# Optimization experiments

Measured on AMD Instinct MI355X. Metric: run time of the kernel, lower is better.

The kernel has to match this reference:

```python
import jax, jax.numpy as jnp
import numpy as np

B, FEAT, Q, L, H_ENC, H_DEC = 256, 64, 16, 2, 128, 256


def _apply_1q(state, U, q):
    # state: [B, 2,2,...,2] (Q qubit axes); U: [B,2,2] complex64
    s = jnp.moveaxis(state, 1 + q, 1)
    shp = s.shape
    s2 = s.reshape(shp[0], 2, -1)
    s2 = jnp.einsum('bij,bjr->bir', U, s2)
    return jnp.moveaxis(s2.reshape(shp), 1, 1 + q)


def _apply_cnot(state, c, t):
    # flip target axis on the control=1 slice
    c0 = jnp.take(state, 0, axis=1 + c)
    c1 = jnp.take(state, 1, axis=1 + c)
    t_ax = 1 + t if t < c else t  # target axis index after removing control axis
    c1 = jnp.flip(c1, axis=t_ax)
    return jnp.stack([c0, c1], axis=1 + c)


def _u3(theta, phi, lam):
    # combined Rz(lam) @ Ry(phi) @ Rx(theta); inputs [B] -> [B,2,2] complex64
    j = jnp.complex64(1j)
    ct, st = jnp.cos(theta / 2), jnp.sin(theta / 2)
    cp, sp = jnp.cos(phi / 2), jnp.sin(phi / 2)
    Rx = jnp.stack([jnp.stack([ct + 0j, -j * st], -1),
                    jnp.stack([-j * st, ct + 0j], -1)], -2)
    Ry = jnp.stack([jnp.stack([cp + 0j, -sp + 0j], -1),
                    jnp.stack([sp + 0j, cp + 0j], -1)], -2)
    em, ep = jnp.exp(-j * lam / 2), jnp.exp(j * lam / 2)
    zero = jnp.zeros_like(em)
    Rz = jnp.stack([jnp.stack([em, zero], -1),
                    jnp.stack([zero, ep], -1)], -2)
    return jnp.einsum('bij,bjk,bkl->bil', Rz, Ry, Rx).astype(jnp.complex64)


def setup_inputs() -> dict:
    key = jax.random.key(0)
    ks = jax.random.split(key, 6)

    def xavier(k, shape):
        lim = float(np.sqrt(6.0 / (shape[0] + shape[1])))
        return jax.random.uniform(k, shape, jnp.float32, -lim, lim)

    return {
        'x': jax.random.normal(ks[0], (B, FEAT), jnp.float32),
        'W1': xavier(ks[1], (FEAT, H_ENC)), 'b1': jnp.zeros((H_ENC,), jnp.float32),
        'W2': xavier(ks[2], (H_ENC, L * Q * 3)), 'b2': jnp.zeros((L * Q * 3,), jnp.float32),
        'scaling': jnp.ones((Q,), jnp.float32),
        'Wd1': xavier(ks[3], (2 ** Q, H_DEC)), 'bd1': jnp.zeros((H_DEC,), jnp.float32),
        'Wd2': xavier(ks[4], (H_DEC, FEAT)), 'bd2': jnp.zeros((FEAT,), jnp.float32),
    }


def reference(x, W1, b1, W2, b2, scaling, Wd1, bd1, Wd2, bd2):
    batch = x.shape[0]
    nq = scaling.shape[0]
    nl = W2.shape[1] // (nq * 3)
    # classical encoder -> quantum rotation angles
    h = jax.nn.relu(x @ W1 + b1)
    p = jnp.tanh(h @ W2 + b2).reshape(batch, nl, nq, 3)
    p = p * scaling[None, None, :, None] * jnp.pi  # theta/phi/lambda scaled by pi
    # batched statevector simulation, |0...0> init
    state = jnp.zeros((batch, 2 ** nq), jnp.complex64).at[:, 0].set(1.0)
    state = state.reshape((batch,) + (2,) * nq)
    for l in range(nl):
        for q in range(nq):
            U = _u3(p[:, l, q, 0], p[:, l, q, 1], p[:, l, q, 2])
            state = _apply_1q(state, U, q)
        if l < nl - 1:
            for q in range(nq - 1):
                state = _apply_cnot(state, q, q + 1)
            state = _apply_cnot(state, nq - 1, 0)
    probs = (jnp.real(state) ** 2 + jnp.imag(state) ** 2).reshape(batch, -1)
    # classical decoder
    out = jax.nn.relu(jax.nn.relu(probs @ Wd1 + bd1) @ Wd2 + bd2)
    return out
```

## Files before the change

kernel.cpp:

```cpp
#include <hip/hip_runtime.h>
#include <hip/hip_fp16.h>

#define PI_F 3.14159265358979323846f

typedef __attribute__((ext_vector_type(8))) _Float16 f16x8;
typedef __attribute__((ext_vector_type(16))) float f32x16;
typedef __attribute__((ext_vector_type(2))) float v2f;

__device__ __forceinline__ v2f pfma(v2f a, v2f b, v2f c) {
    return __builtin_elementwise_fma(a, b, c);
}
__device__ __forceinline__ v2f vswap(v2f a) { return __builtin_shufflevector(a, a, 1, 0); }
__device__ __forceinline__ v2f vsplat(float x) { v2f r; r.x = x; r.y = x; return r; }
__device__ __forceinline__ v2f mkc(v2f u) { v2f r; r.x = -u.y; r.y = u.y; return r; }
__device__ __forceinline__ v2f cmul(v2f a, v2f b) {
    return pfma(mkc(a), vswap(b), vsplat(a.x) * b);
}

__device__ __forceinline__ unsigned f2bf_rn(float x) {
    unsigned u = __float_as_uint(x);
    return (u + 0x7fffu + ((u >> 16) & 1u)) >> 16;
}

union H8 { int4 i4; f16x8 v; };
union U8 { int4 i4; unsigned short u[8]; };

__device__ __forceinline__ void gll16(const void* g, void* l) {
    __builtin_amdgcn_global_load_lds(
        (const __attribute__((address_space(1))) void*)g,
        (__attribute__((address_space(3))) void*)l, 16, 0, 0);
}

struct PreLds {
    float xr[64]; float h[128]; float ang[96];
    v2f vL[32];
    v2f uL[64];
    _Float16 lR[256*8];
    _Float16 lL[512*8];
};

__global__ __launch_bounds__(512) void k_pre(
        const float* __restrict__ x, const float* __restrict__ W1,
        const float* __restrict__ b1, const float* __restrict__ W2,
        const float* __restrict__ b2, const float* __restrict__ scaling,
        _Float16* __restrict__ A) {
    __shared__ PreLds lds;
    const int t = threadIdx.x;
    const int b = blockIdx.x;
    if (t < 64) lds.xr[t] = x[b*64 + t];
    __syncthreads();
    if (t < 128) {
        float acc = b1[t];
        #pragma unroll 8
        for (int f = 0; f < 64; ++f) acc = fmaf(lds.xr[f], W1[f*128 + t], acc);
        lds.h[t] = fmaxf(acc, 0.f);
    }
    __syncthreads();
    if (t < 96) {
        float acc = b2[t];
        #pragma unroll 8
        for (int f = 0; f < 128; ++f) acc = fmaf(lds.h[f], W2[f*96 + t], acc);
        int q = (t/3) & 15;
        lds.ang[t] = tanhf(acc) * scaling[q] * PI_F;
    }
    __syncthreads();
    if (t < 32) {
        int l = t >> 4, q = t & 15;
        const float* a = lds.ang + l*48 + q*3;
        float st, ct, sp, cp, sl, cl;
        sincosf(a[0]*0.5f, &st, &ct);
        sincosf(a[1]*0.5f, &sp, &cp);
        sincosf(a[2]*0.5f, &sl, &cl);
        float2 A00 = make_float2( cp*ct,  sp*st);
        float2 A01 = make_float2(-sp*ct, -cp*st);
        float2 A10 = make_float2( sp*ct, -cp*st);
        float2 A11 = make_float2( cp*ct, -sp*st);
        float2 e0 = make_float2(cl, -sl), e1 = make_float2(cl, sl);
        v2f r00; r00.x = e0.x*A00.x - e0.y*A00.y; r00.y = e0.x*A00.y + e0.y*A00.x;
        v2f r01; r01.x = e0.x*A01.x - e0.y*A01.y; r01.y = e0.x*A01.y + e0.y*A01.x;
        v2f r10; r10.x = e1.x*A10.x - e1.y*A10.y; r10.y = e1.x*A10.y + e1.y*A10.x;
        v2f r11; r11.x = e1.x*A11.x - e1.y*A11.y; r11.y = e1.x*A11.y + e1.y*A11.x;
        if (l == 0) {
            lds.vL[q*2 + 0] = r00;
            lds.vL[q*2 + 1] = r10;
        } else {
            lds.uL[q*4 + 0] = r00; lds.uL[q*4 + 1] = r01;
            lds.uL[q*4 + 2] = r10; lds.uL[q*4 + 3] = r11;
        }
    }
    __syncthreads();
    #define AP(p, s) lds.vL[(15-(p))*2 + (s)]
    #define GG(p, zv, yv) lds.uL[(15-(p))*4 + (zv)*2 + (yv)]
    {
        const float SL = 32.f;
        if (t < 256) {
            v2f Lg[2][2];
            int z0 = t & 1, z1 = (t >> 1) & 1;
            #pragma unroll
            for (int g = 0; g < 2; ++g)
                #pragma unroll
                for (int y = 0; y < 2; ++y)
                    Lg[g][y] = cmul(cmul(GG(0, z0, g), AP(0, g ^ y)), GG(1, z1, y));
            #pragma unroll
            for (int p = 2; p <= 7; ++p) {
                int zp = (t >> p) & 1;
                #pragma unroll
                for (int g = 0; g < 2; ++g) {
                    v2f s0 = cmul(Lg[g][0], AP(p-1, 0)) + cmul(Lg[g][1], AP(p-1, 1));
                    v2f s1 = cmul(Lg[g][0], AP(p-1, 1)) + cmul(Lg[g][1], AP(p-1, 0));
                    Lg[g][0] = cmul(s0, GG(p, zp, 0));
                    Lg[g][1] = cmul(s1, GG(p, zp, 1));
                }
            }
            float lre[4] = {Lg[0][0].x, Lg[0][1].x, Lg[1][0].x, Lg[1][1].x};
            float lim[4] = {Lg[0][0].y, Lg[0][1].y, Lg[1][0].y, Lg[1][1].y};
            H8 hre, him;
            #pragma unroll
            for (int k = 0; k < 4; ++k) {
                hre.v[k]   = (_Float16)(SL * lre[k]);
                hre.v[4+k] = (_Float16)(-SL * lim[k]);
                him.v[k]   = (_Float16)(SL * lim[k]);
                him.v[4+k] = (_Float16)(SL * lre[k]);
            }
            *(int4*)&lds.lL[t*8]         = hre.i4;
            *(int4*)&lds.lL[(256+t)*8]   = him.i4;
        } else {
            const int ts = t - 256;
            v2f Rg[2][2];
            int z15 = (ts >> 7) & 1;
            #pragma unroll
            for (int g = 0; g < 2; ++g)
                #pragma unroll
                for (int y14 = 0; y14 < 2; ++y14)
                    Rg[g][y14] = cmul(cmul(AP(14, y14 ^ g),     AP(15, g)),     GG(15, z15, 0))
                               + cmul(cmul(AP(14, y14 ^ 1 ^ g), AP(15, 1 ^ g)), GG(15, z15, 1));
            #pragma unroll
            for (int p = 14; p >= 8; --p) {
                int zp = (ts >> (p - 8)) & 1;
                #pragma unroll
                for (int g = 0; g < 2; ++g) {
                    v2f t0 = cmul(GG(p, zp, 0), Rg[g][0]);
                    v2f t1 = cmul(GG(p, zp, 1), Rg[g][1]);
                    v2f n0 = cmul(AP(p-1, 0), t0) + cmul(AP(p-1, 1), t1);
                    v2f n1 = cmul(AP(p-1, 1), t0) + cmul(AP(p-1, 0), t1);
                    Rg[g][0] = n0; Rg[g][1] = n1;
                }
            }
            float rre[4] = {Rg[0][0].x, Rg[0][1].x, Rg[1][0].x, Rg[1][1].x};
            float rim[4] = {Rg[0][0].y, Rg[0][1].y, Rg[1][0].y, Rg[1][1].y};
            H8 hr;
            #pragma unroll
            for (int k = 0; k < 4; ++k) {
                hr.v[k]    = (_Float16)(SL * rre[k]);
                hr.v[4+k]  = (_Float16)(SL * rim[k]);
            }
            *(int4*)&lds.lR[ts*8] = hr.i4;
        }
    }
    #undef AP
    #undef GG
    __syncthreads();
    {
        const int wave = t >> 6, lane = t & 63, h2 = lane >> 5, l32 = lane & 31;
        f16x8 zf = {};
        _Float16* Aout = A + ((size_t)b << 16);
        const int zh0 = wave*32;
        f16x8 rf = h2 ? zf : *(const f16x8*)&lds.lR[(zh0 + l32)*8];
        _Float16* rowp = Aout + (size_t)(zh0 + l32)*256 + 4*h2;
        #pragma unroll
        for (int j = 0; j < 8; ++j) {
            f16x8 bre = h2 ? zf : *(const f16x8*)&lds.lL[(j*32 + l32)*8];
            f16x8 bim = h2 ? zf : *(const f16x8*)&lds.lL[(256 + j*32 + l32)*8];
            f32x16 zc = {};
            f32x16 dre = __builtin_amdgcn_mfma_f32_32x32x16_f16(bre, rf, zc, 0, 0, 0);
            f32x16 dim = __builtin_amdgcn_mfma_f32_32x32x16_f16(bim, rf, zc, 0, 0, 0);
            #pragma unroll
            for (int g = 0; g < 4; ++g) {
                union { _Float16 h4[4]; uint2 u2; } pk;
                #pragma unroll
                for (int i = 0; i < 4; ++i) {
                    int q = g*4 + i;
                    float p = fmaf(dre[q], dre[q], dim[q]*dim[q]) * 0.00390625f;
                    pk.h4[i] = (_Float16)p;
                }
                *(uint2*)(rowp + j*32 + 8*g) = pk.u2;
            }
        }
    }
}

__global__ __launch_bounds__(512, 4) void k_gemm(
        const _Float16* __restrict__ A, const float* __restrict__ Wd1,
        unsigned short* __restrict__ partial) {
    __shared__ _Float16 lA[256*64];
    __shared__ _Float16 lB[64*64];
    const int id = blockIdx.x;
    const int xcd = id & 7;
    const int ksg = xcd*16 + ((id >> 3) & 15);
    const int nh  = id >> 7;
    const int k0 = ksg*512, n0 = nh*64;
    const int tid = threadIdx.x;
    const int wave = tid >> 6, lane = tid & 63;
    const int mw = wave >> 1, nw = wave & 1;
    const int h = lane >> 5, l32 = lane & 31;
    const int kw = tid >> 4;
    const int nc4 = (tid & 15) * 4;
    unsigned* lBw = (unsigned*)lB;
    f32x16 acc[2] = {};
    for (int s = 0; s < 8; ++s) {
        const int kb = k0 + s*64;
        const float* wsrc = Wd1 + (size_t)(kb + 2*kw)*256 + n0 + nc4;
        float4 w0 = *(const float4*)(wsrc);
        float4 w1 = *(const float4*)(wsrc + 256);
        #pragma unroll
        for (int i = 0; i < 4; ++i) {
            int ia = wave*4 + i;
            int r = ia*8 + (lane >> 3);
            int cch = (lane & 7) ^ (r & 7);
            gll16(A + (size_t)r*65536 + kb + cch*8, &lA[ia*512]);
        }
        {
            float a0[4] = {w0.x,w0.y,w0.z,w0.w};
            float a1[4] = {w1.x,w1.y,w1.z,w1.w};
            #pragma unroll
            for (int j = 0; j < 4; ++j) {
                int n = nc4 + j;
                int S = ((n >> 3) & 7) ^ (n & 7);
                __half2 hh = __floats2half2_rn(a0[j]*64.f, a1[j]*64.f);
                unsigned u; __builtin_memcpy(&u, &hh, 4);
                lBw[n*32 + (((kw >> 2) ^ S) << 2) + (kw & 3)] = u;
            }
        }
        __syncthreads();
        #pragma unroll
        for (int kk = 0; kk < 4; ++kk) {
            const int ch = kk*2 + h;
            f16x8 af[2], bf;
            #pragma unroll
            for (int xx = 0; xx < 2; ++xx) {
                int rA = mw*64 + xx*32 + l32;
                af[xx] = *(const f16x8*)&lA[rA*64 + ((ch ^ (rA & 7)) << 3)];
            }
            int rB = nw*32 + l32;
            int SB = ((rB >> 3) & 7) ^ (rB & 7);
            bf = *(const f16x8*)&lB[rB*64 + ((ch ^ SB) << 3)];
            #pragma unroll
            for (int i = 0; i < 2; ++i)
                acc[i] = __builtin_amdgcn_mfma_f32_32x32x16_f16(af[i], bf, acc[i], 0, 0, 0);
        }
        __syncthreads();
    }
    #pragma unroll
    for (int i = 0; i < 2; ++i) {
        int n = n0 + nw*32 + l32;
        int mb = mw*64 + i*32 + 4*h;
        #pragma unroll
        for (int q = 0; q < 16; ++q) {
            int m = mb + (q & 3) + 8*(q >> 2);
            partial[((size_t)m*128 + ksg)*256 + n] = (unsigned short)f2bf_rn(acc[i][q]);
        }
    }
}

__global__ __launch_bounds__(256) void k_final(
        const unsigned short* __restrict__ partial, const float* __restrict__ bd1,
        const float* __restrict__ Wd2, const float* __restrict__ bd2,
        float* __restrict__ out) {
    __shared__ float red[8][256];
    __shared__ float row[256];
    __shared__ float red2[4][64];
    const int m = blockIdx.x, t = threadIdx.x;
    const int o = t & 31, kg = t >> 5;
    {
        const unsigned short* p = partial + (size_t)m*32768 + kg*16*256 + o*8;
        float acc[8] = {0.f,0.f,0.f,0.f,0.f,0.f,0.f,0.f};
        #pragma unroll 8
        for (int i = 0; i < 16; ++i) {
            U8 v; v.i4 = *(const int4*)(p + (size_t)i*256);
            #pragma unroll
            for (int j = 0; j < 8; ++j)
                acc[j] += __uint_as_float(((unsigned)v.u[j]) << 16);
        }
        #pragma unroll
        for (int j = 0; j < 8; ++j) red[kg][o*8 + j] = acc[j];
    }
    __syncthreads();
    {
        float s = 0.f;
        #pragma unroll
        for (int g = 0; g < 8; ++g) s += red[g][t];
        const float SC = 1.f / 262144.f;
        row[t] = fmaxf(fmaf(s, SC, bd1[t]), 0.f);
    }
    __syncthreads();
    {
        const int g = t >> 6, tt = t & 63;
        float o2 = 0.f;
        #pragma unroll 8
        for (int i = 0; i < 64; ++i) {
            int n = g*64 + i;
            o2 = fmaf(row[n], Wd2[n*64 + tt], o2);
        }
        red2[g][tt] = o2;
    }
    __syncthreads();
    if (t < 64) {
        float o3 = bd2[t] + ((red2[0][t] + red2[1][t]) + (red2[2][t] + red2[3][t]));
        out[m*64 + t] = fmaxf(o3, 0.f);
    }
}

extern "C" void kernel_launch(void* const* d_in, const int* in_sizes, int n_in,
                              void* d_out, int out_size, void* d_ws, size_t ws_size,
                              hipStream_t stream) {
    const float* x       = (const float*)d_in[0];
    const float* W1      = (const float*)d_in[1];
    const float* b1      = (const float*)d_in[2];
    const float* W2      = (const float*)d_in[3];
    const float* b2      = (const float*)d_in[4];
    const float* scaling = (const float*)d_in[5];
    const float* Wd1     = (const float*)d_in[6];
    const float* bd1     = (const float*)d_in[7];
    const float* Wd2     = (const float*)d_in[8];
    const float* bd2     = (const float*)d_in[9];
    float* out = (float*)d_out;

    char* ws = (char*)d_ws;
    const size_t MB = 1024*1024;
    _Float16* A  = (_Float16*)(ws + 4*MB);
    unsigned short* partial = (unsigned short*)(ws + 36*MB);

    hipLaunchKernelGGL(k_pre, dim3(256), dim3(512), 0, stream,
                       x, W1, b1, W2, b2, scaling, A);
    hipLaunchKernelGGL(k_gemm, dim3(512), dim3(512), 0, stream, A, Wd1, partial);
    hipLaunchKernelGGL(k_final, dim3(256), dim3(256), 0, stream,
                       partial, bd1, Wd2, bd2, out);
}
```

Measured before the change: 159.7 us.

## Use narrower N tiles and longer K splits in decoder GEMM

Changes the split-K GEMM tiling from 64-wide N tiles with 128 K-splits of 512 to 32-wide N tiles with 64 K-splits of 1024. Each wave now computes one 32x32 MFMA tile instead of two. The partial-sum buffer and the final reduction shrink by half. This cuts partial-buffer traffic and reduction work, at the cost of re-reading the A matrix for each of twice as many N tiles and running a longer per-block K loop.

```diff
diff --git a/kernel.cpp b/kernel.cpp
--- a/kernel.cpp
+++ b/kernel.cpp
@@ -193,25 +193,24 @@
         const _Float16* __restrict__ A, const float* __restrict__ Wd1,
         unsigned short* __restrict__ partial) {
     __shared__ _Float16 lA[256*64];
-    __shared__ _Float16 lB[64*64];
+    __shared__ _Float16 lB[32*64];
     const int id = blockIdx.x;
     const int xcd = id & 7;
-    const int ksg = xcd*16 + ((id >> 3) & 15);
-    const int nh  = id >> 7;
-    const int k0 = ksg*512, n0 = nh*64;
+    const int ksg = xcd*8 + ((id >> 3) & 7);
+    const int nh  = id >> 6;
+    const int k0 = ksg*1024, n0 = nh*32;
     const int tid = threadIdx.x;
     const int wave = tid >> 6, lane = tid & 63;
-    const int mw = wave >> 1, nw = wave & 1;
     const int h = lane >> 5, l32 = lane & 31;
     const int kw = tid >> 4;
-    const int nc4 = (tid & 15) * 4;
+    const int nc = (tid & 15) * 2;
     unsigned* lBw = (unsigned*)lB;
-    f32x16 acc[2] = {};
-    for (int s = 0; s < 8; ++s) {
+    f32x16 acc = {};
+    for (int s = 0; s < 16; ++s) {
         const int kb = k0 + s*64;
-        const float* wsrc = Wd1 + (size_t)(kb + 2*kw)*256 + n0 + nc4;
-        float4 w0 = *(const float4*)(wsrc);
-        float4 w1 = *(const float4*)(wsrc + 256);
+        const float* wsrc = Wd1 + (size_t)(kb + 2*kw)*256 + n0 + nc;
+        float2 w0 = *(const float2*)(wsrc);
+        float2 w1 = *(const float2*)(wsrc + 256);
         #pragma unroll
         for (int i = 0; i < 4; ++i) {
             int ia = wave*4 + i;
@@ -220,11 +219,11 @@
             gll16(A + (size_t)r*65536 + kb + cch*8, &lA[ia*512]);
         }
         {
-            float a0[4] = {w0.x,w0.y,w0.z,w0.w};
-            float a1[4] = {w1.x,w1.y,w1.z,w1.w};
-            #pragma unroll
-            for (int j = 0; j < 4; ++j) {
-                int n = nc4 + j;
+            float a0[2] = {w0.x, w0.y};
+            float a1[2] = {w1.x, w1.y};
+            #pragma unroll
+            for (int j = 0; j < 2; ++j) {
+                int n = nc + j;
                 int S = ((n >> 3) & 7) ^ (n & 7);
                 __half2 hh = __floats2half2_rn(a0[j]*64.f, a1[j]*64.f);
                 unsigned u; __builtin_memcpy(&u, &hh, 4);
@@ -235,29 +234,22 @@
         #pragma unroll
         for (int kk = 0; kk < 4; ++kk) {
             const int ch = kk*2 + h;
-            f16x8 af[2], bf;
-            #pragma unroll
-            for (int xx = 0; xx < 2; ++xx) {
-                int rA = mw*64 + xx*32 + l32;
-                af[xx] = *(const f16x8*)&lA[rA*64 + ((ch ^ (rA & 7)) << 3)];
-            }
-            int rB = nw*32 + l32;
+            int rA = wave*32 + l32;
+            f16x8 af = *(const f16x8*)&lA[rA*64 + ((ch ^ (rA & 7)) << 3)];
+            int rB = l32;
             int SB = ((rB >> 3) & 7) ^ (rB & 7);
-            bf = *(const f16x8*)&lB[rB*64 + ((ch ^ SB) << 3)];
-            #pragma unroll
-            for (int i = 0; i < 2; ++i)
-                acc[i] = __builtin_amdgcn_mfma_f32_32x32x16_f16(af[i], bf, acc[i], 0, 0, 0);
+            f16x8 bf = *(const f16x8*)&lB[rB*64 + ((ch ^ SB) << 3)];
+            acc = __builtin_amdgcn_mfma_f32_32x32x16_f16(af, bf, acc, 0, 0, 0);
         }
         __syncthreads();
     }
-    #pragma unroll
-    for (int i = 0; i < 2; ++i) {
-        int n = n0 + nw*32 + l32;
-        int mb = mw*64 + i*32 + 4*h;
+    {
+        int n = n0 + l32;
+        int mb = wave*32 + 4*h;
         #pragma unroll
         for (int q = 0; q < 16; ++q) {
             int m = mb + (q & 3) + 8*(q >> 2);
-            partial[((size_t)m*128 + ksg)*256 + n] = (unsigned short)f2bf_rn(acc[i][q]);
+            partial[((size_t)m*64 + ksg)*256 + n] = (unsigned short)f2bf_rn(acc[q]);
         }
     }
 }
@@ -272,10 +264,10 @@
     const int m = blockIdx.x, t = threadIdx.x;
     const int o = t & 31, kg = t >> 5;
     {
-        const unsigned short* p = partial + (size_t)m*32768 + kg*16*256 + o*8;
+        const unsigned short* p = partial + (size_t)m*16384 + kg*8*256 + o*8;
         float acc[8] = {0.f,0.f,0.f,0.f,0.f,0.f,0.f,0.f};
-        #pragma unroll 8
-        for (int i = 0; i < 16; ++i) {
+        #pragma unroll
+        for (int i = 0; i < 8; ++i) {
             U8 v; v.i4 = *(const int4*)(p + (size_t)i*256);
             #pragma unroll
             for (int j = 0; j < 8; ++j)
```

Measured after the change: 165.5 us. 1.04x slower.
